# Performance work log

Measured on AMD Instinct MI355X. Metric: run time of the kernel, lower is better.

## Reference

```python
import jax, jax.numpy as jnp
import numpy as np

B, N, C, H = 16, 640, 640, 8      # frames, tokens/frame (20*32 latent), channels, heads
D = C // H                        # 80 head dim
N_SEL = 2048                      # number of SACFA-masked tokens gathered across all frames


def setup_inputs() -> dict:
    key = jax.random.key(0)
    ks = jax.random.split(key, 7)
    x = jax.random.normal(ks[0], (B, N, C), jnp.float32)
    s = C ** -0.5
    Wq = jax.random.normal(ks[1], (C, C), jnp.float32) * s
    Wk = jax.random.normal(ks[2], (C, C), jnp.float32) * s
    Wv = jax.random.normal(ks[3], (C, C), jnp.float32) * s
    Wo = jax.random.normal(ks[4], (C, C), jnp.float32) * s
    bo = jnp.zeros((C,), jnp.float32)
    # binary SACFA mask over flattened (B*N) tokens with exactly N_SEL ones
    perm = jax.random.permutation(ks[5], B * N)
    sacfa_mask = jnp.zeros((B * N,), jnp.float32).at[perm[:N_SEL]].set(1.0)
    return {"x": x, "Wq": Wq, "Wk": Wk, "Wv": Wv, "Wo": Wo, "bo": bo,
            "sacfa_mask": sacfa_mask, "n_sel": N_SEL}


def reference(x, Wq, Wk, Wv, Wo, bo, sacfa_mask, n_sel):
    b, n, c = x.shape
    h = H
    d = c // h
    # QKV projections (self-attention: context = x)
    q = x @ Wq
    k = x @ Wk
    v = x @ Wv
    # SACFA: gather boolean-masked tokens from all frames (static count n_sel)
    sel = jnp.nonzero(sacfa_mask > 0.5, size=n_sel)[0]           # [n_sel]
    k_tok = k.reshape(b * n, c)[sel]                              # [n_sel, c]
    v_tok = v.reshape(b * n, c)[sel]
    # repeat shared tokens per frame and concat along kv sequence
    k = jnp.concatenate([k, jnp.broadcast_to(k_tok, (b, n_sel, c))], axis=1)
    v = jnp.concatenate([v, jnp.broadcast_to(v_tok, (b, n_sel, c))], axis=1)
    # head split: b s (h d) -> b h s d
    to_heads = lambda t: t.reshape(b, -1, h, d).transpose(0, 2, 1, 3)
    qh, kh, vh = to_heads(q), to_heads(k), to_heads(v)
    # scaled dot-product attention (math of xformers memory_efficient_attention)
    scores = jnp.einsum('bhqd,bhkd->bhqk', qh, kh) * (d ** -0.5)  # [b,h,n,n+n_sel]
    attn = jax.nn.softmax(scores, axis=-1)
    out = jnp.einsum('bhqk,bhkd->bhqd', attn, vh)
    out = out.transpose(0, 2, 1, 3).reshape(b, n, c)              # b h n d -> b n c
    return out @ Wo + bo
```

## Files before the change

### kernel.cpp

```cpp
#include <hip/hip_runtime.h>
#include <hip/hip_bf16.h>

#define B_    16
#define N_    640
#define C_    640
#define H_    8
#define D_    80
#define DP_   96
#define CP_   768
#define NSEL_ 2048
#define NTOK_ 10240
#define NKV_  12288

typedef short bf16x8 __attribute__((ext_vector_type(8)));
typedef float f32x4  __attribute__((ext_vector_type(4)));
typedef unsigned int u32;
typedef u32 u32x4 __attribute__((ext_vector_type(4)));
typedef unsigned short u16;

#define MFMA16(a,b,c) __builtin_amdgcn_mfma_f32_16x16x32_bf16((a),(b),(c),0,0,0)

static __device__ __forceinline__ u16 f2b(float f) {
  u32 x = __builtin_bit_cast(u32, f);
  x += 0x7fffu + ((x >> 16) & 1u);
  return (u16)(x >> 16);
}

static __device__ __forceinline__ u32 cvtpk(float lo, float hi) {
  u32 r;
  asm("v_cvt_pk_bf16_f32 %0, %1, %2" : "=v"(r) : "v"(lo), "v"(hi));
  return r;
}

static __device__ __forceinline__ void gl16(const void* g, void* l) {
  __builtin_amdgcn_global_load_lds((const __attribute__((address_space(1))) u32*)g,
                                   (__attribute__((address_space(3))) u32*)l, 16, 0, 0);
}

static __device__ __forceinline__ int PI(int r) {
  return ((r >> 2) & 3) * 8 + (r >> 5) * 32 + ((r >> 4) & 1) * 4 + (r & 3);
}

__global__ __launch_bounds__(256) void k_convert_x(const float* __restrict__ x,
                                                   u16* __restrict__ xb) {
  int i = blockIdx.x * 256 + threadIdx.x;
  float4 v = ((const float4*)x)[i];
  ushort4 o;
  o.x = f2b(v.x); o.y = f2b(v.y); o.z = f2b(v.z); o.w = f2b(v.w);
  ((ushort4*)xb)[i] = o;
}

__global__ __launch_bounds__(256) void k_convert_w(const float* w0, const float* w1,
                                                   const float* w2, const float* w3,
                                                   u16* t0, u16* t1, u16* t2, u16* t3) {
  const float* W = (blockIdx.z == 0) ? w0 : (blockIdx.z == 1) ? w1 : (blockIdx.z == 2) ? w2 : w3;
  u16*         T = (blockIdx.z == 0) ? t0 : (blockIdx.z == 1) ? t1 : (blockIdx.z == 2) ? t2 : t3;
  __shared__ float tile[32][33];
  int tx = threadIdx.x & 31, ty = threadIdx.x >> 5;
  int n0 = blockIdx.x * 32, k0 = blockIdx.y * 32;
#pragma unroll
  for (int r = 0; r < 4; r++)
    tile[ty + 8 * r][tx] = W[(k0 + ty + 8 * r) * C_ + n0 + tx];
  __syncthreads();
#pragma unroll
  for (int r = 0; r < 4; r++)
    T[(n0 + ty + 8 * r) * C_ + k0 + tx] = f2b(tile[tx][ty + 8 * r]);
}

__global__ __launch_bounds__(1024) void k_scan(const float* __restrict__ mask,
                                               int* __restrict__ sel) {
  __shared__ int wcnt[16];
  __shared__ int carry;
  int tid = threadIdx.x, lane = tid & 63, wid = tid >> 6;
  float v[10];
#pragma unroll
  for (int r = 0; r < 10; r++) v[r] = mask[r * 1024 + tid];
  if (tid == 0) carry = 0;
  __syncthreads();
  for (int r = 0; r < 10; r++) {
    bool p = v[r] > 0.5f;
    unsigned long long b = __ballot(p);
    if (lane == 0) wcnt[wid] = __popcll(b);
    __syncthreads();
    int off = carry;
    for (int w = 0; w < wid; w++) off += wcnt[w];
    if (p) sel[off + __popcll(b & ((1ull << lane) - 1ull))] = r * 1024 + tid;
    __syncthreads();
    if (tid == 0) {
      int s = 0;
      for (int w = 0; w < 16; w++) s += wcnt[w];
      carry += s;
    }
    __syncthreads();
  }
}

#define QSCALE_ (1.4426950408889634f * 0.11180339887498949f)

__global__ __launch_bounds__(256) void k_gemm_qkv(const u16* __restrict__ A,
                                                  const u16* __restrict__ WkT,
                                                  const u16* __restrict__ WvT,
                                                  const u16* __restrict__ WqT,
                                                  u16* __restrict__ Kp,
                                                  u16* __restrict__ Vt,
                                                  u16* __restrict__ Qp) {
  __shared__ u16 lA[128 * 32];
  __shared__ u16 lB[128 * 32];
  int tid = threadIdx.x, lane = tid & 63, wid = tid >> 6;
  int l15 = lane & 15, l4 = lane >> 4;
  int f = blockIdx.x;
  int which = f / 400, g = f % 400;
  const u16* BT = (which == 0) ? WkT : (which == 1) ? WvT : WqT;
  int m0 = (g % 80) * 128, n0 = (g / 80) * 128;
  int wr = wid >> 1, wc = wid & 1;
  int tok = tid >> 2, ch = tid & 3;
  int sc = ch ^ (tok & 3);
  f32x4 acc[4][4];
#pragma unroll
  for (int mi = 0; mi < 4; mi++)
#pragma unroll
    for (int ni = 0; ni < 4; ni++) acc[mi][ni] = (f32x4){0.f, 0.f, 0.f, 0.f};

  for (int k0 = 0; k0 < C_; k0 += 32) {
    __syncthreads();
    gl16(A  + (m0 + tok)      * C_ + k0 + sc * 8, (char*)lA + tid * 16);
    gl16(A  + (m0 + tok + 64) * C_ + k0 + sc * 8, (char*)lA + 4096 + tid * 16);
    gl16(BT + (n0 + tok)      * C_ + k0 + sc * 8, (char*)lB + tid * 16);
    gl16(BT + (n0 + tok + 64) * C_ + k0 + sc * 8, (char*)lB + 4096 + tid * 16);
    __syncthreads();
    bf16x8 af[4], bfr[4];
#pragma unroll
    for (int mi = 0; mi < 4; mi++) {
      int r = wr * 64 + mi * 16 + l15;
      af[mi] = *(const bf16x8*)((const char*)lA + r * 64 + ((l4 ^ (r & 3)) * 16));
    }
#pragma unroll
    for (int ni = 0; ni < 4; ni++) {
      int r = wc * 64 + ni * 16 + l15;
      bfr[ni] = *(const bf16x8*)((const char*)lB + r * 64 + ((l4 ^ (r & 3)) * 16));
    }
#pragma unroll
    for (int mi = 0; mi < 4; mi++)
#pragma unroll
      for (int ni = 0; ni < 4; ni++) acc[mi][ni] = MFMA16(af[mi], bfr[ni], acc[mi][ni]);
  }

  int cbase = n0 + wc * 64, rbase = m0 + wr * 64;
  if (which == 1) {
#pragma unroll
    for (int mi = 0; mi < 4; mi++)
#pragma unroll
      for (int ni = 0; ni < 4; ni++) {
        int c = cbase + ni * 16 + l15;
        int r0 = rbase + mi * 16 + l4 * 4;
        ushort4 pk;
        pk.x = f2b(acc[mi][ni][0]); pk.y = f2b(acc[mi][ni][1]);
        pk.z = f2b(acc[mi][ni][2]); pk.w = f2b(acc[mi][ni][3]);
        *(ushort4*)(Vt + c * NKV_ + r0) = pk;
      }
  } else {
    u16* P = (which == 0) ? Kp : Qp;
    float sc2 = (which == 2) ? QSCALE_ : 1.f;
#pragma unroll
    for (int mi = 0; mi < 4; mi++)
#pragma unroll
      for (int ni = 0; ni < 4; ni++) {
        int c = cbase + ni * 16 + l15;
        int h = c / 80, d = c % 80;
#pragma unroll
        for (int rg = 0; rg < 4; rg++) {
          int r = rbase + mi * 16 + l4 * 4 + rg;
          P[r * CP_ + h * DP_ + d] = f2b(acc[mi][ni][rg] * sc2);
        }
      }
  }
}

__global__ __launch_bounds__(256) void k_gemm_o(const u16* __restrict__ A,
                                                const u16* __restrict__ BT,
                                                float* __restrict__ out,
                                                const float* __restrict__ bias) {
  __shared__ u16 lA[128 * 32];
  __shared__ u16 lB[128 * 32];
  int tid = threadIdx.x, lane = tid & 63, wid = tid >> 6;
  int l15 = lane & 15, l4 = lane >> 4;
  int f = blockIdx.x;
  int m0 = (f % 80) * 128, n0 = (f / 80) * 128;
  int wr = wid >> 1, wc = wid & 1;
  int tok = tid >> 2, ch = tid & 3;
  int sc = ch ^ (tok & 3);
  f32x4 acc[4][4];
#pragma unroll
  for (int mi = 0; mi < 4; mi++)
#pragma unroll
    for (int ni = 0; ni < 4; ni++) acc[mi][ni] = (f32x4){0.f, 0.f, 0.f, 0.f};

  for (int k0 = 0; k0 < C_; k0 += 32) {
    __syncthreads();
    gl16(A  + (m0 + tok)      * C_ + k0 + sc * 8, (char*)lA + tid * 16);
    gl16(A  + (m0 + tok + 64) * C_ + k0 + sc * 8, (char*)lA + 4096 + tid * 16);
    gl16(BT + (n0 + tok)      * C_ + k0 + sc * 8, (char*)lB + tid * 16);
    gl16(BT + (n0 + tok + 64) * C_ + k0 + sc * 8, (char*)lB + 4096 + tid * 16);
    __syncthreads();
    bf16x8 af[4], bfr[4];
#pragma unroll
    for (int mi = 0; mi < 4; mi++) {
      int r = wr * 64 + mi * 16 + l15;
      af[mi] = *(const bf16x8*)((const char*)lA + r * 64 + ((l4 ^ (r & 3)) * 16));
    }
#pragma unroll
    for (int ni = 0; ni < 4; ni++) {
      int r = wc * 64 + ni * 16 + l15;
      bfr[ni] = *(const bf16x8*)((const char*)lB + r * 64 + ((l4 ^ (r & 3)) * 16));
    }
#pragma unroll
    for (int mi = 0; mi < 4; mi++)
#pragma unroll
      for (int ni = 0; ni < 4; ni++) acc[mi][ni] = MFMA16(af[mi], bfr[ni], acc[mi][ni]);
  }

  int cbase = n0 + wc * 64, rbase = m0 + wr * 64;
#pragma unroll
  for (int ni = 0; ni < 4; ni++) {
    int c = cbase + ni * 16 + l15;
    float bv = bias[c];
#pragma unroll
    for (int mi = 0; mi < 4; mi++)
#pragma unroll
      for (int rg = 0; rg < 4; rg++)
        out[(rbase + mi * 16 + l4 * 4 + rg) * C_ + c] = acc[mi][ni][rg] + bv;
  }
}

__global__ __launch_bounds__(256) void k_gather(const int* __restrict__ sel,
                                                u16* __restrict__ Kp,
                                                u16* __restrict__ Vt) {
  int i = blockIdx.x;
  int t = threadIdx.x;
  int s = sel[i];
  const u32* src = (const u32*)(Kp + s * CP_);
  u32* dst = (u32*)(Kp + (NTOK_ + i) * CP_);
  dst[t] = src[t];
  if (t < 128) dst[256 + t] = src[256 + t];
  for (int c = t; c < C_; c += 256)
    Vt[c * NKV_ + NTOK_ + i] = Vt[c * NKV_ + s];
}

__global__ __launch_bounds__(256, 2) void k_attn(const u16* __restrict__ Qp,
                                                 const u16* __restrict__ Kp,
                                                 const u16* __restrict__ Vt,
                                                 u16* __restrict__ Ob) {
  __shared__ u16 smem[3][10240];
  int tid = threadIdx.x, lane = tid & 63, wid = tid >> 6;
  int l15 = lane & 15, l4 = lane >> 4;
  int f = blockIdx.x;
  int b = f & 15, h = (f >> 4) & 7, qt = f >> 7;
  int q0 = qt * 128 + wid * 32;
  const int NT = 42;
  const bf16x8 kz = {0, 0, 0, 0, 0, 0, 0, 0};

  bf16x8 qf[2][2], qtl[2];
#pragma unroll
  for (int m = 0; m < 2; m++) {
    const u16* qrow = Qp + (size_t)(b * N_ + q0 + m * 16 + l15) * CP_ + h * DP_;
#pragma unroll
    for (int kk = 0; kk < 2; kk++)
      qf[m][kk] = *(const bf16x8*)(qrow + kk * 32 + l4 * 8);
    qtl[m] = (l4 < 2) ? *(const bf16x8*)(qrow + 64 + l4 * 8) : kz;
  }

  f32x4 o[2][5];
#pragma unroll
  for (int m = 0; m < 2; m++)
#pragma unroll
    for (int d5 = 0; d5 < 5; d5++) o[m][d5] = (f32x4){0.f, 0.f, 0.f, 0.f};
  float li_[2] = {0.f, 0.f};

  u32 gof[5];
#pragma unroll
  for (int k = 0; k < 5; k++) {
    int s = tid + 256 * k;
    if (s < 512) {
      int kk = s >> 8, rem = s & 255, tok = rem >> 2, c = rem & 3;
      gof[k] = (u32)(PI(tok) * CP_ + h * DP_ + kk * 32 + ((c ^ (tok & 3)) * 8));
    } else if (s < 640) {
      int j = s - 512, tok = j >> 1, ch = j & 1;
      gof[k] = (u32)(PI(tok) * CP_ + h * DP_ + 64 + ch * 8);
    } else {
      int j = s - 640, vd = j >> 3, c = j & 7;
      gof[k] = (u32)((h * D_ + vd) * NKV_ + ((c ^ (vd & 7)) * 8));
    }
  }

  auto stage = [&](int g, int buf) {
    int tokbase = (g < 10) ? (b * N_ + g * 64) : (NTOK_ + (g - 10) * 64);
    size_t kadd = (size_t)tokbase * CP_;
    char* dst = (char*)smem[buf] + tid * 16;
#pragma unroll
    for (int k = 0; k < 5; k++) {
      bool isv = (k >= 3) || (k == 2 && tid >= 128);
      const u16* src = isv ? (Vt + gof[k] + tokbase) : (Kp + gof[k] + kadd);
      gl16(src, dst + k * 4096);
    }
  };

  stage(0, 0);
  stage(1, 1);
  asm volatile("s_waitcnt vmcnt(5)" ::: "memory");
  __builtin_amdgcn_sched_barrier(0);
  __builtin_amdgcn_s_barrier();
  __builtin_amdgcn_sched_barrier(0);

  for (int tt = 0; tt < NT; tt++) {
    const char* kb0 = (const char*)smem[tt % 3];
    const char* vb0 = kb0 + 10240;
    if (tt + 2 < NT) stage(tt + 2, (tt + 2) % 3);

    bf16x8 kb[12];
#pragma unroll
    for (int kk = 0; kk < 2; kk++)
#pragma unroll
      for (int nt = 0; nt < 4; nt++) {
        int tk = nt * 16 + l15;
        kb[kk * 4 + nt] = *(const bf16x8*)(kb0 + kk * 4096 + tk * 64 + ((l4 ^ (tk & 3)) * 16));
      }
#pragma unroll
    for (int nt = 0; nt < 4; nt++) {
      int tk = nt * 16 + l15;
      bf16x8 t = *(const bf16x8*)(kb0 + 8192 + tk * 32 + ((l4 & 1) * 16));
      kb[8 + nt] = (l4 < 2) ? t : kz;
    }
    bf16x8 vb[10];
#pragma unroll
    for (int kk2 = 0; kk2 < 2; kk2++)
#pragma unroll
      for (int d5 = 0; d5 < 5; d5++) {
        int dd = d5 * 16 + l15;
        vb[kk2 * 5 + d5] =
            *(const bf16x8*)(vb0 + dd * 128 + (((kk2 * 4 + l4) ^ (dd & 7)) * 16));
      }

    f32x4 s[2][4];
#pragma unroll
    for (int m = 0; m < 2; m++)
#pragma unroll
      for (int nt = 0; nt < 4; nt++) s[m][nt] = (f32x4){0.f, 0.f, 0.f, 0.f};
    __builtin_amdgcn_s_setprio(1);
#pragma unroll
    for (int kk = 0; kk < 2; kk++)
#pragma unroll
      for (int nt = 0; nt < 4; nt++) {
        s[0][nt] = MFMA16(kb[kk * 4 + nt], qf[0][kk], s[0][nt]);
        s[1][nt] = MFMA16(kb[kk * 4 + nt], qf[1][kk], s[1][nt]);
      }
#pragma unroll
    for (int nt = 0; nt < 4; nt++) {
      s[0][nt] = MFMA16(kb[8 + nt], qtl[0], s[0][nt]);
      s[1][nt] = MFMA16(kb[8 + nt], qtl[1], s[1][nt]);
    }
    __builtin_amdgcn_s_setprio(0);

#pragma unroll
    for (int m = 0; m < 2; m++) {
#pragma unroll
      for (int nt = 0; nt < 4; nt++)
#pragma unroll
        for (int rg = 0; rg < 4; rg++)
          s[m][nt][rg] = exp2f(s[m][nt][rg]);
      f32x4 ps = (s[m][0] + s[m][1]) + (s[m][2] + s[m][3]);
      li_[m] += (ps[0] + ps[1]) + (ps[2] + ps[3]);
    }

    bf16x8 pa[2][2];
#pragma unroll
    for (int m = 0; m < 2; m++)
#pragma unroll
      for (int kk2 = 0; kk2 < 2; kk2++) {
        u32x4 w;
        w.x = cvtpk(s[m][2 * kk2][0],     s[m][2 * kk2][1]);
        w.y = cvtpk(s[m][2 * kk2][2],     s[m][2 * kk2][3]);
        w.z = cvtpk(s[m][2 * kk2 + 1][0], s[m][2 * kk2 + 1][1]);
        w.w = cvtpk(s[m][2 * kk2 + 1][2], s[m][2 * kk2 + 1][3]);
        pa[m][kk2] = __builtin_bit_cast(bf16x8, w);
      }

    __builtin_amdgcn_s_setprio(1);
#pragma unroll
    for (int kk2 = 0; kk2 < 2; kk2++)
#pragma unroll
      for (int d5 = 0; d5 < 5; d5++) {
        o[0][d5] = MFMA16(pa[0][kk2], vb[kk2 * 5 + d5], o[0][d5]);
        o[1][d5] = MFMA16(pa[1][kk2], vb[kk2 * 5 + d5], o[1][d5]);
      }
    __builtin_amdgcn_s_setprio(0);

    if (tt + 2 < NT) {
      asm volatile("s_waitcnt vmcnt(5)" ::: "memory");
    } else {
      asm volatile("s_waitcnt vmcnt(0)" ::: "memory");
    }
    __builtin_amdgcn_sched_barrier(0);
    __builtin_amdgcn_s_barrier();
    __builtin_amdgcn_sched_barrier(0);
  }

#pragma unroll
  for (int m = 0; m < 2; m++) {
    li_[m] += __shfl_xor(li_[m], 16);
    li_[m] += __shfl_xor(li_[m], 32);
  }
#pragma unroll
  for (int m = 0; m < 2; m++)
#pragma unroll
    for (int rg = 0; rg < 4; rg++) {
      float lv = __shfl(li_[m], l4 * 4 + rg);
      float inv = 1.f / lv;
#pragma unroll
      for (int d5 = 0; d5 < 5; d5++) {
        int r = b * N_ + q0 + m * 16 + l4 * 4 + rg;
        Ob[(size_t)r * C_ + h * D_ + d5 * 16 + l15] = f2b(o[m][d5][rg] * inv);
      }
    }
}

extern "C" void kernel_launch(void* const* d_in, const int* in_sizes, int n_in,
                              void* d_out, int out_size, void* d_ws, size_t ws_size,
                              hipStream_t stream) {
  (void)in_sizes; (void)n_in; (void)out_size; (void)ws_size;
  const float* x    = (const float*)d_in[0];
  const float* Wq   = (const float*)d_in[1];
  const float* Wk   = (const float*)d_in[2];
  const float* Wv   = (const float*)d_in[3];
  const float* Wo   = (const float*)d_in[4];
  const float* bo   = (const float*)d_in[5];
  const float* mask = (const float*)d_in[6];

  char* ws = (char*)d_ws;
  u16* xb  = (u16*)(ws + 0);
  u16* Ob  = xb;
  u16* WqT = (u16*)(ws + 13107200);
  u16* WkT = (u16*)(ws + 13926400);
  u16* WvT = (u16*)(ws + 14745600);
  u16* WoT = (u16*)(ws + 15564800);
  u16* Qp  = (u16*)(ws + 16384000);
  u16* Kp  = (u16*)(ws + 32112640);
  u16* Vt  = (u16*)(ws + 50987008);
  int* sel = (int*)(ws + 66715648);

  k_convert_x<<<6400, 256, 0, stream>>>(x, xb);
  k_convert_w<<<dim3(20, 20, 4), 256, 0, stream>>>(Wq, Wk, Wv, Wo, WqT, WkT, WvT, WoT);
  k_scan<<<1, 1024, 0, stream>>>(mask, sel);
  k_gemm_qkv<<<1200, 256, 0, stream>>>(xb, WkT, WvT, WqT, Kp, Vt, Qp);
  k_gather<<<2048, 256, 0, stream>>>(sel, Kp, Vt);
  k_attn<<<640, 256, 0, stream>>>(Qp, Kp, Vt, Ob);
  k_gemm_o<<<400, 256, 0, stream>>>(Ob, WoT, (float*)d_out, bo);
}
```

Before: 238.1 us.

## Double-buffer attention K/V staging for 3 blocks/CU and use K16 MFMA for head tail

The attention kernel drops from triple to double-buffered LDS staging of K/V tiles, with a plain block barrier per iteration. That lowers LDS per block so the launch bound can request 3 resident blocks per CU instead of 2. Separately, the 16-wide remainder of the 80-dim head product now uses a 16x16x16 bf16 MFMA on 4-element fragments when the builtin exists, instead of a zero-padded 16x16x32 MFMA. The trade-off is less prefetch depth (only one tile in flight), a full vmcnt drain at each barrier, and tighter register limits that could cause spilling.

After: 231.7 us. 2.7% less time.

```diff
diff --git a/kernel.cpp b/kernel.cpp
--- a/kernel.cpp
+++ b/kernel.cpp
@@ -13,12 +13,23 @@
 #define NKV_  12288
 
 typedef short bf16x8 __attribute__((ext_vector_type(8)));
+typedef short bf16x4 __attribute__((ext_vector_type(4)));
 typedef float f32x4  __attribute__((ext_vector_type(4)));
 typedef unsigned int u32;
 typedef u32 u32x4 __attribute__((ext_vector_type(4)));
 typedef unsigned short u16;
 
 #define MFMA16(a,b,c) __builtin_amdgcn_mfma_f32_16x16x32_bf16((a),(b),(c),0,0,0)
+
+#if defined(__has_builtin)
+#if __has_builtin(__builtin_amdgcn_mfma_f32_16x16x16bf16_1k)
+#define HAVE_TAIL16 1
+#define MFMA16K16(a,b,c) __builtin_amdgcn_mfma_f32_16x16x16bf16_1k((a),(b),(c),0,0,0)
+#endif
+#endif
+#ifndef HAVE_TAIL16
+#define HAVE_TAIL16 0
+#endif
 
 static __device__ __forceinline__ u16 f2b(float f) {
   u32 x = __builtin_bit_cast(u32, f);
@@ -246,11 +257,11 @@
     Vt[c * NKV_ + NTOK_ + i] = Vt[c * NKV_ + s];
 }
 
-__global__ __launch_bounds__(256, 2) void k_attn(const u16* __restrict__ Qp,
+__global__ __launch_bounds__(256, 3) void k_attn(const u16* __restrict__ Qp,
                                                  const u16* __restrict__ Kp,
                                                  const u16* __restrict__ Vt,
                                                  u16* __restrict__ Ob) {
-  __shared__ u16 smem[3][10240];
+  __shared__ u16 smem[2][10240];
   int tid = threadIdx.x, lane = tid & 63, wid = tid >> 6;
   int l15 = lane & 15, l4 = lane >> 4;
   int f = blockIdx.x;
@@ -259,14 +270,23 @@
   const int NT = 42;
   const bf16x8 kz = {0, 0, 0, 0, 0, 0, 0, 0};
 
-  bf16x8 qf[2][2], qtl[2];
+  bf16x8 qf[2][2];
+#if HAVE_TAIL16
+  bf16x4 qtl[2];
+#else
+  bf16x8 qtl[2];
+#endif
 #pragma unroll
   for (int m = 0; m < 2; m++) {
     const u16* qrow = Qp + (size_t)(b * N_ + q0 + m * 16 + l15) * CP_ + h * DP_;
 #pragma unroll
     for (int kk = 0; kk < 2; kk++)
       qf[m][kk] = *(const bf16x8*)(qrow + kk * 32 + l4 * 8);
+#if HAVE_TAIL16
+    qtl[m] = *(const bf16x4*)(qrow + 64 + l4 * 4);
+#else
     qtl[m] = (l4 < 2) ? *(const bf16x8*)(qrow + 64 + l4 * 8) : kz;
+#endif
   }
 
   f32x4 o[2][5];
@@ -305,18 +325,15 @@
   };
 
   stage(0, 0);
-  stage(1, 1);
-  asm volatile("s_waitcnt vmcnt(5)" ::: "memory");
-  __builtin_amdgcn_sched_barrier(0);
-  __builtin_amdgcn_s_barrier();
-  __builtin_amdgcn_sched_barrier(0);
+  __syncthreads();
+  int cur = 0;
 
   for (int tt = 0; tt < NT; tt++) {
-    const char* kb0 = (const char*)smem[tt % 3];
+    if (tt + 1 < NT) stage(tt + 1, cur ^ 1);
+    const char* kb0 = (const char*)smem[cur];
     const char* vb0 = kb0 + 10240;
-    if (tt + 2 < NT) stage(tt + 2, (tt + 2) % 3);
-
-    bf16x8 kb[12];
+
+    bf16x8 kb[8];
 #pragma unroll
     for (int kk = 0; kk < 2; kk++)
 #pragma unroll
@@ -324,12 +341,22 @@
         int tk = nt * 16 + l15;
         kb[kk * 4 + nt] = *(const bf16x8*)(kb0 + kk * 4096 + tk * 64 + ((l4 ^ (tk & 3)) * 16));
       }
+#if HAVE_TAIL16
+    bf16x4 kt[4];
+#pragma unroll
+    for (int nt = 0; nt < 4; nt++) {
+      int tk = nt * 16 + l15;
+      kt[nt] = *(const bf16x4*)(kb0 + 8192 + tk * 32 + l4 * 8);
+    }
+#else
+    bf16x8 kt[4];
 #pragma unroll
     for (int nt = 0; nt < 4; nt++) {
       int tk = nt * 16 + l15;
       bf16x8 t = *(const bf16x8*)(kb0 + 8192 + tk * 32 + ((l4 & 1) * 16));
-      kb[8 + nt] = (l4 < 2) ? t : kz;
-    }
+      kt[nt] = (l4 < 2) ? t : kz;
+    }
+#endif
     bf16x8 vb[10];
 #pragma unroll
     for (int kk2 = 0; kk2 < 2; kk2++)
@@ -355,8 +382,13 @@
       }
 #pragma unroll
     for (int nt = 0; nt < 4; nt++) {
-      s[0][nt] = MFMA16(kb[8 + nt], qtl[0], s[0][nt]);
-      s[1][nt] = MFMA16(kb[8 + nt], qtl[1], s[1][nt]);
+#if HAVE_TAIL16
+      s[0][nt] = MFMA16K16(kt[nt], qtl[0], s[0][nt]);
+      s[1][nt] = MFMA16K16(kt[nt], qtl[1], s[1][nt]);
+#else
+      s[0][nt] = MFMA16(kt[nt], qtl[0], s[0][nt]);
+      s[1][nt] = MFMA16(kt[nt], qtl[1], s[1][nt]);
+#endif
     }
     __builtin_amdgcn_s_setprio(0);
 
@@ -394,14 +426,8 @@
       }
     __builtin_amdgcn_s_setprio(0);
 
-    if (tt + 2 < NT) {
-      asm volatile("s_waitcnt vmcnt(5)" ::: "memory");
-    } else {
-      asm volatile("s_waitcnt vmcnt(0)" ::: "memory");
-    }
-    __builtin_amdgcn_sched_barrier(0);
-    __builtin_amdgcn_s_barrier();
-    __builtin_amdgcn_sched_barrier(0);
+    __syncthreads();
+    cur ^= 1;
   }
 
 #pragma unroll
```
